# Optimization experiments

Hardware: AMD Instinct MI355X
Metric: run time of the kernel (lower is better)

## Reference

```python
import jax, jax.numpy as jnp
import numpy as np
import math

B, T, E, H, L, FF = 8, 512, 1024, 16, 4, 4096
D = E // H
LN_EPS = 1e-5


def _layernorm(x, g, b):
    mu = jnp.mean(x, axis=-1, keepdims=True)
    var = jnp.mean((x - mu) ** 2, axis=-1, keepdims=True)
    return (x - mu) * jax.lax.rsqrt(var + LN_EPS) * g + b


def setup_inputs() -> dict:
    key = jax.random.key(0)
    ks = jax.random.split(key, 16)
    s = 0.02
    return {
        "src": jax.random.normal(ks[0], (B, T, E), jnp.float32),
        "in_proj_w": jax.random.normal(ks[1], (L, 3 * E, E), jnp.float32) * s,
        "in_proj_b": jax.random.normal(ks[2], (L, 3 * E), jnp.float32) * s,
        "out_w": jax.random.normal(ks[3], (L, E, E), jnp.float32) * s,
        "out_b": jnp.zeros((L, E), jnp.float32),
        "ff1_w": jax.random.normal(ks[4], (L, FF, E), jnp.float32) * s,
        "ff1_b": jnp.zeros((L, FF), jnp.float32),
        "ff2_w": jax.random.normal(ks[5], (L, E, FF), jnp.float32) * s,
        "ff2_b": jnp.zeros((L, E), jnp.float32),
        "ln1_g": jnp.ones((L, E), jnp.float32),
        "ln1_b": jnp.zeros((L, E), jnp.float32),
        "ln2_g": jnp.ones((L, E), jnp.float32),
        "ln2_b": jnp.zeros((L, E), jnp.float32),
        "head_w": jax.random.normal(ks[6], (1, E), jnp.float32) * s,
        "head_b": jnp.zeros((1,), jnp.float32),
    }


def reference(src, in_proj_w, in_proj_b, out_w, out_b, ff1_w, ff1_b,
              ff2_w, ff2_b, ln1_g, ln1_b, ln2_g, ln2_b, head_w, head_b):
    b, t, e = src.shape
    # --- PositionalEncoding (faithful to batch_first bug: pe indexed by batch dim) ---
    pos = jnp.arange(b, dtype=jnp.float32)[:, None]            # [B,1]
    div = jnp.exp(jnp.arange(0, e, 2, dtype=jnp.float32) * (-math.log(10000.0) / e))
    pe = jnp.zeros((b, e), jnp.float32)
    pe = pe.at[:, 0::2].set(jnp.sin(pos * div)).at[:, 1::2].set(jnp.cos(pos * div))
    x = src + pe[:, None, :]                                   # broadcast over seq

    # --- Gaussian bias, shared across layers (Tq == Tk == T) ---
    dist = jnp.arange(t)[:, None] - jnp.arange(t)[None, :]
    gb = jnp.exp(-(dist.astype(jnp.float32) ** 2) / (2.0 * (t / 4.0) ** 2))  # [T,T]

    for l in range(L):
        qkv = x @ in_proj_w[l].T + in_proj_b[l]                # [B,T,3E]
        q, k, v = jnp.split(qkv, 3, axis=-1)
        q = q.reshape(b, t, H, D).transpose(0, 2, 1, 3)        # [B,H,T,D]
        k = k.reshape(b, t, H, D).transpose(0, 2, 1, 3)
        v = v.reshape(b, t, H, D).transpose(0, 2, 1, 3)
        scores = jnp.einsum("bhqd,bhkd->bhqk", q, k) / math.sqrt(D)
        w = jax.nn.softmax(scores, axis=-1)                    # [B,H,Tq,Tk]
        w = w * gb[None, None]
        w = w / (jnp.sum(w, axis=-1, keepdims=True) + 1e-5)
        o = jnp.einsum("bhqk,bhkd->bhqd", w, v)
        o = o.transpose(0, 2, 1, 3).reshape(b, t, e)
        o = o @ out_w[l].T + out_b[l]
        x = _layernorm(x + o, ln1_g[l], ln1_b[l])              # post-norm
        ff = jax.nn.relu(x @ ff1_w[l].T + ff1_b[l]) @ ff2_w[l].T + ff2_b[l]
        x = _layernorm(x + ff, ln2_g[l], ln2_b[l])

    last = x[:, -1, :]                                         # [B,E]
    return last @ head_w.T + head_b                            # [B,1]
```

## Files before the change

### kernel.cpp

```cpp
#include <hip/hip_runtime.h>

typedef unsigned short u16;
typedef __attribute__((ext_vector_type(4))) float v4f;
typedef __attribute__((ext_vector_type(8))) short v8bf;

extern "C" __device__ float __ocml_native_exp2_f32(float);
__device__ inline float ex2(float x){ return __ocml_native_exp2_f32(x); }

__device__ inline u16 f2bf(float f){
  union { float f; unsigned u; } v; v.f = f;
  unsigned r = (v.u + 0x7FFFu + ((v.u >> 16) & 1u)) >> 16;
  return (u16)r;
}
__device__ inline float bf2f(u16 u){
  union { unsigned u; float f; } v; v.u = ((unsigned)u) << 16;
  return v.f;
}

#define GLD_LDS16(gp, lp) \
  __builtin_amdgcn_global_load_lds((const __attribute__((address_space(1))) void*)(gp), \
                                   (__attribute__((address_space(3))) void*)(lp), 16, 0, 0)
#define VMCNT(n) asm volatile("s_waitcnt vmcnt(" #n ")" ::: "memory")
#define LGKM0 do { asm volatile("s_waitcnt lgkmcnt(0)" ::: "memory"); \
                   __builtin_amdgcn_sched_barrier(0); } while (0)

template<int FUSE>
__global__ __launch_bounds__(512, 2) void gemm9(
    const u16* __restrict__ A, const u16* __restrict__ W,
    const float* __restrict__ bias, void* __restrict__ C,
    int N, int K, int Kc, int gx, int gy)
{
  __shared__ u16 smem[65536];
  const int tid = threadIdx.x, lane = tid & 63, wid = tid >> 6;
  const int wm = wid >> 2, wn = wid & 3;

  const int nwg = gridDim.x, bid = blockIdx.x;
  const int swz = (bid & 7) * (nwg >> 3) + (bid >> 3);
  const int gxy = gx * gy;
  const int bz = swz / gxy;
  const int rem = swz - bz * gxy;
  const int by = rem / gx;
  const int bx = rem - by * gx;
  const int k0 = bz * Kc;
  const int NT = Kc >> 6;

  const int arow = (wid >> 1) * 16 + (lane & 15);
  const int akk  = (wid & 1) * 32 + ((lane >> 4) << 3);
  const u16* gA = A + (size_t)(by * 256 + arow) * K + k0 + akk;
  const u16* gB = W + (size_t)(bx * 256 + arow) * K + k0 + akk;
  u16* ldst = smem + tid * 8;

  auto stageA = [&](int t, int h) {
    u16* d = ldst + (t & 1) * 32768 + h * 8192;
    const u16* s = gA + (size_t)(h * 128) * K + t * 64;
    GLD_LDS16(s, d);
    GLD_LDS16(s + (size_t)64 * K, d + 4096);
  };
  auto stageB = [&](int t, int h) {
    u16* d = ldst + (t & 1) * 32768 + (2 + h) * 8192;
    const u16* s = gB + (size_t)(h * 128) * K + t * 64;
    GLD_LDS16(s, d);
    GLD_LDS16(s + (size_t)64 * K, d + 4096);
  };

  v4f acc[8][4];
  #pragma unroll
  for (int i = 0; i < 8; ++i)
    #pragma unroll
    for (int j = 0; j < 4; ++j) acc[i][j] = (v4f){0.f, 0.f, 0.f, 0.f};

  stageA(0, 0); stageA(0, 1); stageB(0, 0); stageB(0, 1);
  if (NT > 1) { stageA(1, 0); stageA(1, 1); VMCNT(4); } else { VMCNT(0); }
  __builtin_amdgcn_s_barrier();

  const u16* rdA = smem + wm * 8192 + lane * 8;
  const u16* rdB = smem + 16384 + (wn >> 1) * 8192 + lane * 8;
  const int jb = (wn & 1) * 4;

  v8bf aq[4][2], bq[4][2];

#define MFMA_CL(QI, NLO)                                                        \
  do {                                                                          \
    __builtin_amdgcn_s_setprio(1);                                              \
    _Pragma("unroll") for (int m = 0; m < 4; ++m)                               \
      _Pragma("unroll") for (int n = NLO; n < NLO + 2; ++n)                     \
        _Pragma("unroll") for (int kk = 0; kk < 2; ++kk)                        \
          acc[(QI)*4 + m][n] = __builtin_amdgcn_mfma_f32_16x16x32_bf16(         \
              aq[m][kk], bq[n][kk], acc[(QI)*4 + m][n], 0, 0, 0);               \
    __builtin_amdgcn_s_setprio(0);                                              \
  } while (0)

  for (int t = 0; t < NT; ++t) {
    const int bufo = (t & 1) * 32768;
    __builtin_amdgcn_sched_barrier(0);
    #pragma unroll
    for (int m = 0; m < 4; ++m)
      #pragma unroll
      for (int kk = 0; kk < 2; ++kk)
        aq[m][kk] = *(const v8bf*)(rdA + bufo + (m * 2 + kk) * 512);
    #pragma unroll
    for (int n = 0; n < 2; ++n)
      #pragma unroll
      for (int kk = 0; kk < 2; ++kk)
        bq[n][kk] = *(const v8bf*)(rdB + bufo + ((jb + n) * 2 + kk) * 512);
    if (t + 1 < NT) stageB(t + 1, 0);
    MFMA_CL(0, 0);
    #pragma unroll
    for (int n = 2; n < 4; ++n)
      #pragma unroll
      for (int kk = 0; kk < 2; ++kk)
        bq[n][kk] = *(const v8bf*)(rdB + bufo + ((jb + n) * 2 + kk) * 512);
    if (t + 1 < NT) stageB(t + 1, 1);
    MFMA_CL(0, 2);
    __builtin_amdgcn_s_barrier();
    __builtin_amdgcn_sched_barrier(0);
    #pragma unroll
    for (int m = 0; m < 4; ++m)
      #pragma unroll
      for (int kk = 0; kk < 2; ++kk)
        aq[m][kk] = *(const v8bf*)(rdA + bufo + ((4 + m) * 2 + kk) * 512);
    if (t + 2 < NT) stageA(t + 2, 0);
    MFMA_CL(1, 2);
    __builtin_amdgcn_s_barrier();
    __builtin_amdgcn_sched_barrier(0);
    if (t + 2 < NT) stageA(t + 2, 1);
    MFMA_CL(1, 0);
    if (t < NT - 2) { VMCNT(4); } else if (t == NT - 2) { VMCNT(0); }
    __builtin_amdgcn_s_barrier();
  }
#undef MFMA_CL

  const int cn0 = bx * 256 + wn * 64 + (lane & 15);
  const int rm0 = by * 256 + wm * 128 + ((lane >> 4) << 2);
  if (FUSE == 2) {
    u16* Cp = (u16*)C + (size_t)bz * 4096 * N;
    #pragma unroll
    for (int i = 0; i < 8; ++i)
      #pragma unroll
      for (int r = 0; r < 4; ++r) {
        size_t ro = (size_t)(rm0 + i * 16 + r) * N + cn0;
        #pragma unroll
        for (int j = 0; j < 4; ++j) Cp[ro + j * 16] = f2bf(acc[i][j][r]);
      }
  } else {
    float bv[4];
    #pragma unroll
    for (int j = 0; j < 4; ++j) bv[j] = bias[cn0 + j * 16];
    u16* Cp = (u16*)C;
    #pragma unroll
    for (int i = 0; i < 8; ++i)
      #pragma unroll
      for (int r = 0; r < 4; ++r) {
        size_t ro = (size_t)(rm0 + i * 16 + r) * N + cn0;
        #pragma unroll
        for (int j = 0; j < 4; ++j) {
          float v = acc[i][j][r] + bv[j];
          if (FUSE == 1) v = fmaxf(v, 0.f);
          Cp[ro + j * 16] = f2bf(v);
        }
      }
  }
}

__global__ __launch_bounds__(256, 2) void attn_f(const u16* __restrict__ qkv,
                                                 u16* __restrict__ o)
{
  __shared__ u16 Kf[2][4096];
  __shared__ u16 Vt[2][4096];
  __shared__ u16 wbuf[64 * 72];
  const int tid = threadIdx.x, lane = tid & 63, wid = tid >> 6;
  const int grp = lane >> 4, li = lane & 15;
  const int bh = blockIdx.y, b = bh >> 4, h = bh & 15;
  const int q0 = blockIdx.x * 64;
  const u16* Qg = qkv + (size_t)b * 512 * 3072 + h * 64;
  const u16* Kg = Qg + 1024;
  const u16* Vg = Qg + 2048;

  const size_t qrow = (size_t)(q0 + wid * 16 + li) * 3072;
  v8bf qa0 = *(const v8bf*)(Qg + qrow + grp * 8);
  v8bf qa1 = *(const v8bf*)(Qg + qrow + 32 + grp * 8);

  const u16* kga = Kg + (size_t)(wid * 16 + li) * 3072 + grp * 8;
  auto k_stage = [&](int kt, int buf) {
    #pragma unroll
    for (int s = 0; s < 2; ++s)
      GLD_LDS16(kga + (size_t)kt * 64 * 3072 + s * 32, &Kf[buf][(wid * 2 + s) * 512]);
  };
  auto v_load = [&](int kt, int x) -> v8bf {
    int u = x * 256 + tid, kk = u >> 3, d0 = (u & 7) * 8;
    return *(const v8bf*)(Vg + (size_t)(kt * 64 + kk) * 3072 + d0);
  };
  auto vt_write = [&](int buf, int x, v8bf v) {
    int u = x * 256 + tid, kk = u >> 3, d0 = (u & 7) * 8;
    int kg = (kk >> 3) & 3, kks = kk >> 5, jb2 = (kk & 7) * 2;
    #pragma unroll
    for (int i = 0; i < 8; ++i) {
      int d = d0 + i;
      int byte = (((d >> 4) * 2 + kks) * 1024 + ((d & 15) + 16 * kg) * 16 + jb2)
                 ^ (((d >> 4) & 3) << 5);
      *(u16*)((char*)&Vt[buf][0] + byte) = (u16)v[i];
    }
  };

  v4f oacc[4];
  #pragma unroll
  for (int nt = 0; nt < 4; ++nt) oacc[nt] = (v4f){0.f, 0.f, 0.f, 0.f};
  float mreg[4] = {-1e30f, -1e30f, -1e30f, -1e30f};
  float sgl[4] = {0.f, 0.f, 0.f, 0.f};
  float fqv[4];
  #pragma unroll
  for (int j = 0; j < 4; ++j) fqv[j] = (float)(q0 + wid * 16 + grp * 4 + j);

  v8bf vst[2][2];
  k_stage(0, 0);
  k_stage(1, 1);
  vst[0][0] = v_load(0, 0); vst[0][1] = v_load(0, 1);
  VMCNT(0);
  vt_write(0, 0, vst[0][0]); vt_write(0, 1, vst[0][1]);
  vst[1][0] = v_load(1, 0); vst[1][1] = v_load(1, 1);
  LGKM0;
  __builtin_amdgcn_s_barrier();

  const float SC2 = 0.18033688011112042f;
  const float GC2 = 4.4027559280058695e-05f;

  #pragma unroll
  for (int t = 0; t < 8; ++t) {
    const int cur = t & 1;
    v8bf bq0[4], bq1[4];
    #pragma unroll
    for (int nb = 0; nb < 4; ++nb) {
      bq0[nb] = *(const v8bf*)&Kf[cur][(nb * 2 + 0) * 512 + lane * 8];
      bq1[nb] = *(const v8bf*)&Kf[cur][(nb * 2 + 1) * 512 + lane * 8];
    }
    v4f pa[4];
    #pragma unroll
    for (int nb = 0; nb < 4; ++nb) {
      v4f z = (v4f){0.f, 0.f, 0.f, 0.f};
      z = __builtin_amdgcn_mfma_f32_16x16x32_bf16(qa0, bq0[nb], z, 0, 0, 0);
      pa[nb] = __builtin_amdgcn_mfma_f32_16x16x32_bf16(qa1, bq1[nb], z, 0, 0, 0);
    }
    if (t < 7) {
      __builtin_amdgcn_s_barrier();
      __builtin_amdgcn_sched_barrier(0);
      if (t + 2 < 8) k_stage(t + 2, cur);
      if (t < 6) { VMCNT(2); } else { VMCNT(0); }
      vt_write((t + 1) & 1, 0, vst[(t + 1) & 1][0]);
      vt_write((t + 1) & 1, 1, vst[(t + 1) & 1][1]);
      if (t + 2 < 8) { vst[t & 1][0] = v_load(t + 2, 0); vst[t & 1][1] = v_load(t + 2, 1); }
    }
    #pragma unroll
    for (int nb = 0; nb < 4; ++nb) {
      const float fk = (float)(t * 64 + nb * 16 + li);
      #pragma unroll
      for (int j = 0; j < 4; ++j) {
        float d = fqv[j] - fk;
        pa[nb][j] = pa[nb][j] * SC2 - d * d * GC2;
      }
    }
    float rel = -1e30f;
    #pragma unroll
    for (int j = 0; j < 4; ++j)
      #pragma unroll
      for (int nb = 0; nb < 4; ++nb)
        rel = fmaxf(rel, pa[nb][j] - mreg[j]);
    if (!__all(rel <= 11.0f)) {
      #pragma unroll
      for (int j = 0; j < 4; ++j) {
        float tmax = fmaxf(fmaxf(pa[0][j], pa[1][j]), fmaxf(pa[2][j], pa[3][j]));
        tmax = fmaxf(tmax, __shfl_xor(tmax, 1));
        tmax = fmaxf(tmax, __shfl_xor(tmax, 2));
        tmax = fmaxf(tmax, __shfl_xor(tmax, 4));
        tmax = fmaxf(tmax, __shfl_xor(tmax, 8));
        float mn = fmaxf(mreg[j], tmax);
        float sc = ex2(mreg[j] - mn);
        mreg[j] = mn;
        sgl[j] *= sc;
        #pragma unroll
        for (int nt = 0; nt < 4; ++nt) oacc[nt][j] *= sc;
      }
    }
    #pragma unroll
    for (int j = 0; j < 4; ++j) {
      #pragma unroll
      for (int nb = 0; nb < 4; ++nb) {
        float e = ex2(pa[nb][j] - mreg[j]);
        pa[nb][j] = e;
        sgl[j] += e;
      }
    }
    #pragma unroll
    for (int j = 0; j < 4; ++j) {
      const int row = wid * 16 + grp * 4 + j;
      #pragma unroll
      for (int nb = 0; nb < 4; ++nb) {
        union { float f; unsigned u; } cv; cv.f = pa[nb][j];
        wbuf[row * 72 + ((nb * 16 + li) ^ (grp << 3))] = (u16)(cv.u >> 16);
      }
    }
    const int swr = ((li >> 2) & 3) << 3;
    v8bf af0 = *(const v8bf*)&wbuf[(wid * 16 + li) * 72 + ((0 * 32 + grp * 8) ^ swr)];
    v8bf af1 = *(const v8bf*)&wbuf[(wid * 16 + li) * 72 + ((1 * 32 + grp * 8) ^ swr)];
    #pragma unroll
    for (int nt = 0; nt < 4; ++nt) {
      v8bf bv0 = *(const v8bf*)((char*)&Vt[cur][0] + ((((nt * 2 + 0) * 1024) + lane * 16) ^ ((nt & 3) << 5)));
      v8bf bv1 = *(const v8bf*)((char*)&Vt[cur][0] + ((((nt * 2 + 1) * 1024) + lane * 16) ^ ((nt & 3) << 5)));
      oacc[nt] = __builtin_amdgcn_mfma_f32_16x16x32_bf16(af0, bv0, oacc[nt], 0, 0, 0);
      oacc[nt] = __builtin_amdgcn_mfma_f32_16x16x32_bf16(af1, bv1, oacc[nt], 0, 0, 0);
    }
    if (t < 7) {
      if (t < 6) { VMCNT(2); } else { VMCNT(0); }
      LGKM0;
      __builtin_amdgcn_s_barrier();
      __builtin_amdgcn_sched_barrier(0);
    }
  }

  float rin[4];
  #pragma unroll
  for (int j = 0; j < 4; ++j) {
    float s = sgl[j];
    s += __shfl_xor(s, 1); s += __shfl_xor(s, 2);
    s += __shfl_xor(s, 4); s += __shfl_xor(s, 8);
    rin[j] = 1.f / s;
  }
  const size_t obase = (size_t)(b * 512 + q0 + wid * 16 + grp * 4) * 1024 + h * 64;
  #pragma unroll
  for (int nt = 0; nt < 4; ++nt)
    #pragma unroll
    for (int j = 0; j < 4; ++j)
      o[obase + (size_t)j * 1024 + nt * 16 + li] = f2bf(oacc[nt][j] * rin[j]);
}

__global__ __launch_bounds__(256) void ln_res4_k(
    const u16* __restrict__ x, const u16* __restrict__ part,
    const float* __restrict__ bias, const float* __restrict__ g,
    const float* __restrict__ beta, u16* __restrict__ yb)
{
  const int row = blockIdx.x, tid = threadIdx.x;
  const size_t base = (size_t)row * 1024 + tid * 4;
  const size_t MN = 4096ull * 1024;
  ushort4 xv = *(const ushort4*)(x + base);
  const int e = tid * 4;
  float4 bb = *(const float4*)(bias + e);
  float v0 = bf2f(xv.x) + bb.x, v1 = bf2f(xv.y) + bb.y;
  float v2 = bf2f(xv.z) + bb.z, v3 = bf2f(xv.w) + bb.w;
  #pragma unroll
  for (int q = 0; q < 4; ++q) {
    ushort4 pv = *(const ushort4*)(part + q * MN + base);
    v0 += bf2f(pv.x); v1 += bf2f(pv.y); v2 += bf2f(pv.z); v3 += bf2f(pv.w);
  }
  float s = v0 + v1 + v2 + v3;
  float q2 = v0*v0 + v1*v1 + v2*v2 + v3*v3;
  #pragma unroll
  for (int m = 1; m < 64; m <<= 1) { s += __shfl_xor(s, m); q2 += __shfl_xor(q2, m); }
  __shared__ float ls[4], lq[4];
  if ((tid & 63) == 0) { ls[tid >> 6] = s; lq[tid >> 6] = q2; }
  __syncthreads();
  s = ls[0] + ls[1] + ls[2] + ls[3];
  q2 = lq[0] + lq[1] + lq[2] + lq[3];
  const float mu = s * (1.f / 1024.f);
  const float var = q2 * (1.f / 1024.f) - mu * mu;
  const float rs = rsqrtf(var + 1e-5f);
  float4 gv = *(const float4*)(g + e);
  float4 be = *(const float4*)(beta + e);
  float o0 = (v0 - mu) * rs * gv.x + be.x;
  float o1 = (v1 - mu) * rs * gv.y + be.y;
  float o2 = (v2 - mu) * rs * gv.z + be.z;
  float o3 = (v3 - mu) * rs * gv.w + be.w;
  ushort4 ob; ob.x = f2bf(o0); ob.y = f2bf(o1); ob.z = f2bf(o2); ob.w = f2bf(o3);
  *(ushort4*)(yb + base) = ob;
}

__global__ __launch_bounds__(256) void pe_add_k(const float* __restrict__ src,
    u16* __restrict__ xb)
{
  const int u = blockIdx.x * 256 + threadIdx.x;
  const int e4 = (u & 255) * 4;
  const int b = u >> 17;
  const float C = -18.420680743952367f * (1.f / 1024.f);
  float4 sv = ((const float4*)src)[u];
  float fb = (float)b;
  float fr0 = __expf((float)(e4 >> 1) * C);
  float fr1 = __expf((float)((e4 >> 1) + 1) * C);
  float a0 = fb * fr0, a1 = fb * fr1;
  ushort4 ov;
  ov.x = f2bf(sv.x + __sinf(a0));
  ov.y = f2bf(sv.y + __cosf(a0));
  ov.z = f2bf(sv.z + __sinf(a1));
  ov.w = f2bf(sv.w + __cosf(a1));
  ((ushort4*)xb)[u] = ov;
}

__global__ __launch_bounds__(256) void cvt4_k(const float* __restrict__ s0,
    const float* __restrict__ s1, const float* __restrict__ s2,
    const float* __restrict__ s3, u16* __restrict__ dst)
{
  int i = blockIdx.x * 256 + threadIdx.x;
  const float* s; size_t off;
  if (i < 786432)       { s = s0; off = (size_t)i; }
  else if (i < 1048576) { s = s1; off = (size_t)i - 786432; }
  else if (i < 2097152) { s = s2; off = (size_t)i - 1048576; }
  else                  { s = s3; off = (size_t)i - 2097152; }
  float4 v = ((const float4*)s)[off];
  ushort4 ov; ov.x = f2bf(v.x); ov.y = f2bf(v.y); ov.z = f2bf(v.z); ov.w = f2bf(v.w);
  ((ushort4*)dst)[i] = ov;
}

__global__ __launch_bounds__(256) void head_k(const u16* __restrict__ xb,
    const float* __restrict__ hw, const float* __restrict__ hb, float* __restrict__ out)
{
  const int b = blockIdx.x, tid = threadIdx.x;
  const ushort4 xv = ((const ushort4*)(xb + ((size_t)b * 512 + 511) * 1024))[tid];
  const float4 wv = ((const float4*)hw)[tid];
  float s = bf2f(xv.x) * wv.x + bf2f(xv.y) * wv.y + bf2f(xv.z) * wv.z + bf2f(xv.w) * wv.w;
  #pragma unroll
  for (int m = 1; m < 64; m <<= 1) s += __shfl_xor(s, m);
  __shared__ float ls[4];
  if ((tid & 63) == 0) ls[tid >> 6] = s;
  __syncthreads();
  if (tid == 0) out[b] = ls[0] + ls[1] + ls[2] + ls[3] + hb[0];
}

extern "C" void kernel_launch(void* const* d_in, const int* in_sizes, int n_in,
                              void* d_out, int out_size, void* d_ws, size_t ws_size,
                              hipStream_t stream)
{
  const float* src  = (const float*)d_in[0];
  const float* ipw  = (const float*)d_in[1];
  const float* ipb  = (const float*)d_in[2];
  const float* outw = (const float*)d_in[3];
  const float* outb = (const float*)d_in[4];
  const float* f1w  = (const float*)d_in[5];
  const float* f1b  = (const float*)d_in[6];
  const float* f2w  = (const float*)d_in[7];
  const float* f2b  = (const float*)d_in[8];
  const float* l1g  = (const float*)d_in[9];
  const float* l1b  = (const float*)d_in[10];
  const float* l2g  = (const float*)d_in[11];
  const float* l2b  = (const float*)d_in[12];
  const float* hw   = (const float*)d_in[13];
  const float* hb   = (const float*)d_in[14];

  char* p = (char*)d_ws;
  auto take = [&](size_t bytes) { char* r = p; p += (bytes + 255) & ~(size_t)255; return r; };
  u16*   xb   = (u16*)  take(4096ull * 1024 * 2);
  u16*   slA  = (u16*)  take(4096ull * 4096 * 2);
  u16*   ob   = (u16*)  take(4096ull * 1024 * 2);
  u16*   pf   = (u16*)  take(4ull * 4096 * 1024 * 2);
  u16*   wc   = (u16*)  take(12582912ull * 2);

  u16* qkvb = slA;
  u16* f1o  = slA;

  pe_add_k<<<4096, 256, 0, stream>>>(src, xb);

  for (int l = 0; l < 4; ++l) {
    cvt4_k<<<12288, 256, 0, stream>>>(ipw + (size_t)l * 3145728,
                                      outw + (size_t)l * 1048576,
                                      f1w + (size_t)l * 4194304,
                                      f2w + (size_t)l * 4194304, wc);
    gemm9<0><<<192, 512, 0, stream>>>(xb, wc, ipb + l * 3072, qkvb, 3072, 1024, 1024, 12, 16);
    attn_f<<<dim3(8, 128), 256, 0, stream>>>(qkvb, ob);
    gemm9<2><<<256, 512, 0, stream>>>(ob, wc + 3145728, nullptr, pf, 1024, 1024, 256, 4, 16);
    ln_res4_k<<<4096, 256, 0, stream>>>(xb, pf, outb + l * 1024, l1g + l * 1024, l1b + l * 1024, xb);
    gemm9<1><<<256, 512, 0, stream>>>(xb, wc + 4194304, f1b + l * 4096, f1o, 4096, 1024, 1024, 16, 16);
    gemm9<2><<<256, 512, 0, stream>>>(f1o, wc + 8388608, nullptr, pf, 1024, 4096, 1024, 4, 16);
    ln_res4_k<<<4096, 256, 0, stream>>>(xb, pf, f2b + l * 1024, l2g + l * 1024, l2b + l * 1024, xb);
  }
  head_k<<<8, 256, 0, stream>>>(xb, hw, hb, (float*)d_out);
}
```

Before: 822.1 us.

## Restructure GEMM main loop into ping-pong quadrant schedule with register-prefetched LDS reads

Replaces the GEMM main loop with a two-tile unrolled schedule. Each quarter step issues its MFMA block while the LDS fragments for the next quadrant are read into a separate B register set, and global-to-LDS staging for tile t+2 is spread across the quarters. Both buffers are prefilled up front and vmcnt waits are tuned. The aim is to hide LDS read latency behind matrix math. In exchange it needs more barriers, more registers, and an even tile count of at least two per block.

```diff
diff --git a/kernel.cpp b/kernel.cpp
--- a/kernel.cpp
+++ b/kernel.cpp
@@ -25,7 +25,7 @@
                    __builtin_amdgcn_sched_barrier(0); } while (0)
 
 template<int FUSE>
-__global__ __launch_bounds__(512, 2) void gemm9(
+__global__ __launch_bounds__(512, 2) void gemm10(
     const u16* __restrict__ A, const u16* __restrict__ W,
     const float* __restrict__ bias, void* __restrict__ C,
     int N, int K, int Kc, int gx, int gy)
@@ -43,6 +43,7 @@
   const int bx = rem - by * gx;
   const int k0 = bz * Kc;
   const int NT = Kc >> 6;
+  const int NI = NT >> 1;
 
   const int arow = (wid >> 1) * 16 + (lane & 15);
   const int akk  = (wid & 1) * 32 + ((lane >> 4) << 3);
@@ -70,65 +71,81 @@
     for (int j = 0; j < 4; ++j) acc[i][j] = (v4f){0.f, 0.f, 0.f, 0.f};
 
   stageA(0, 0); stageA(0, 1); stageB(0, 0); stageB(0, 1);
-  if (NT > 1) { stageA(1, 0); stageA(1, 1); VMCNT(4); } else { VMCNT(0); }
+  stageA(1, 0); stageA(1, 1); stageB(1, 0); stageB(1, 1);
+  VMCNT(0);
   __builtin_amdgcn_s_barrier();
 
   const u16* rdA = smem + wm * 8192 + lane * 8;
   const u16* rdB = smem + 16384 + (wn >> 1) * 8192 + lane * 8;
   const int jb = (wn & 1) * 4;
 
-  v8bf aq[4][2], bq[4][2];
-
-#define MFMA_CL(QI, NLO)                                                        \
-  do {                                                                          \
-    __builtin_amdgcn_s_setprio(1);                                              \
-    _Pragma("unroll") for (int m = 0; m < 4; ++m)                               \
-      _Pragma("unroll") for (int n = NLO; n < NLO + 2; ++n)                     \
-        _Pragma("unroll") for (int kk = 0; kk < 2; ++kk)                        \
-          acc[(QI)*4 + m][n] = __builtin_amdgcn_mfma_f32_16x16x32_bf16(         \
-              aq[m][kk], bq[n][kk], acc[(QI)*4 + m][n], 0, 0, 0);               \
-    __builtin_amdgcn_s_setprio(0);                                              \
+  v8bf aq[4][2];
+  v8bf bq[2][2][2];
+
+#define READ_A(HALF, BO)                                                        \
+  do { _Pragma("unroll") for (int m = 0; m < 4; ++m)                            \
+         _Pragma("unroll") for (int kk = 0; kk < 2; ++kk)                       \
+           aq[m][kk] = *(const v8bf*)(rdA + (BO) + (((HALF)*4 + m)*2 + kk)*512);\
   } while (0)
-
-  for (int t = 0; t < NT; ++t) {
-    const int bufo = (t & 1) * 32768;
-    __builtin_amdgcn_sched_barrier(0);
-    #pragma unroll
-    for (int m = 0; m < 4; ++m)
-      #pragma unroll
-      for (int kk = 0; kk < 2; ++kk)
-        aq[m][kk] = *(const v8bf*)(rdA + bufo + (m * 2 + kk) * 512);
-    #pragma unroll
-    for (int n = 0; n < 2; ++n)
-      #pragma unroll
-      for (int kk = 0; kk < 2; ++kk)
-        bq[n][kk] = *(const v8bf*)(rdB + bufo + ((jb + n) * 2 + kk) * 512);
-    if (t + 1 < NT) stageB(t + 1, 0);
-    MFMA_CL(0, 0);
-    #pragma unroll
-    for (int n = 2; n < 4; ++n)
-      #pragma unroll
-      for (int kk = 0; kk < 2; ++kk)
-        bq[n][kk] = *(const v8bf*)(rdB + bufo + ((jb + n) * 2 + kk) * 512);
-    if (t + 1 < NT) stageB(t + 1, 1);
-    MFMA_CL(0, 2);
-    __builtin_amdgcn_s_barrier();
-    __builtin_amdgcn_sched_barrier(0);
-    #pragma unroll
-    for (int m = 0; m < 4; ++m)
-      #pragma unroll
-      for (int kk = 0; kk < 2; ++kk)
-        aq[m][kk] = *(const v8bf*)(rdA + bufo + ((4 + m) * 2 + kk) * 512);
-    if (t + 2 < NT) stageA(t + 2, 0);
-    MFMA_CL(1, 2);
-    __builtin_amdgcn_s_barrier();
-    __builtin_amdgcn_sched_barrier(0);
-    if (t + 2 < NT) stageA(t + 2, 1);
-    MFMA_CL(1, 0);
-    if (t < NT - 2) { VMCNT(4); } else if (t == NT - 2) { VMCNT(0); }
-    __builtin_amdgcn_s_barrier();
-  }
-#undef MFMA_CL
+#define READ_B(QJ, BO)                                                          \
+  do { _Pragma("unroll") for (int n = 0; n < 2; ++n)                            \
+         _Pragma("unroll") for (int kk = 0; kk < 2; ++kk)                       \
+           bq[QJ][n][kk] = *(const v8bf*)(rdB + (BO) + ((jb + (QJ)*2 + n)*2 + kk)*512); \
+  } while (0)
+#define MFMA_Q(QI, QJ)                                                          \
+  do { __builtin_amdgcn_s_setprio(1);                                           \
+       _Pragma("unroll") for (int m = 0; m < 4; ++m)                            \
+         _Pragma("unroll") for (int n = 0; n < 2; ++n)                          \
+           _Pragma("unroll") for (int kk = 0; kk < 2; ++kk)                     \
+             acc[(QI)*4 + m][(QJ)*2 + n] =                                      \
+               __builtin_amdgcn_mfma_f32_16x16x32_bf16(aq[m][kk], bq[QJ][n][kk],\
+                   acc[(QI)*4 + m][(QJ)*2 + n], 0, 0, 0);                       \
+       __builtin_amdgcn_s_setprio(0);                                           \
+  } while (0)
+#define BAR __builtin_amdgcn_s_barrier()
+
+  READ_A(0, 0);
+  READ_B(0, 0);
+
+  for (int i = 0; i < NI - 1; ++i) {
+    const int t2 = 2 * i + 2, t3 = 2 * i + 3;
+    LGKM0; MFMA_Q(0, 0);
+    READ_B(1, 0);
+    BAR;
+    LGKM0; MFMA_Q(0, 1);
+    READ_A(1, 0); stageA(t2, 0); stageB(t2, 0);
+    BAR;
+    LGKM0; MFMA_Q(1, 0); VMCNT(6);
+    READ_B(0, 32768); stageB(t2, 1);
+    BAR;
+    LGKM0; MFMA_Q(1, 1); VMCNT(6);
+    READ_A(0, 32768); stageA(t2, 1);
+    BAR;
+    LGKM0; MFMA_Q(0, 0);
+    READ_B(1, 32768);
+    BAR;
+    LGKM0; MFMA_Q(0, 1);
+    READ_A(1, 32768); stageA(t3, 0); stageB(t3, 0);
+    BAR;
+    LGKM0; MFMA_Q(1, 0); VMCNT(6);
+    READ_B(0, 0); stageB(t3, 1);
+    BAR;
+    LGKM0; MFMA_Q(1, 1); VMCNT(6);
+    READ_A(0, 0); stageA(t3, 1);
+    BAR;
+  }
+  LGKM0; MFMA_Q(0, 0); READ_B(1, 0); BAR;
+  LGKM0; MFMA_Q(0, 1); READ_A(1, 0); BAR;
+  LGKM0; MFMA_Q(1, 0); VMCNT(0); READ_B(0, 32768); BAR;
+  LGKM0; MFMA_Q(1, 1); READ_A(0, 32768); BAR;
+  LGKM0; MFMA_Q(0, 0); READ_B(1, 32768); BAR;
+  LGKM0; MFMA_Q(0, 1); READ_A(1, 32768); BAR;
+  LGKM0; MFMA_Q(1, 0); BAR;
+  LGKM0; MFMA_Q(1, 1);
+#undef READ_A
+#undef READ_B
+#undef MFMA_Q
+#undef BAR
 
   const int cn0 = bx * 256 + wn * 64 + (lane & 15);
   const int rm0 = by * 256 + wm * 128 + ((lane >> 4) << 2);
@@ -460,12 +477,12 @@
                                       outw + (size_t)l * 1048576,
                                       f1w + (size_t)l * 4194304,
                                       f2w + (size_t)l * 4194304, wc);
-    gemm9<0><<<192, 512, 0, stream>>>(xb, wc, ipb + l * 3072, qkvb, 3072, 1024, 1024, 12, 16);
+    gemm10<0><<<192, 512, 0, stream>>>(xb, wc, ipb + l * 3072, qkvb, 3072, 1024, 1024, 12, 16);
     attn_f<<<dim3(8, 128), 256, 0, stream>>>(qkvb, ob);
-    gemm9<2><<<256, 512, 0, stream>>>(ob, wc + 3145728, nullptr, pf, 1024, 1024, 256, 4, 16);
+    gemm10<2><<<256, 512, 0, stream>>>(ob, wc + 3145728, nullptr, pf, 1024, 1024, 256, 4, 16);
     ln_res4_k<<<4096, 256, 0, stream>>>(xb, pf, outb + l * 1024, l1g + l * 1024, l1b + l * 1024, xb);
-    gemm9<1><<<256, 512, 0, stream>>>(xb, wc + 4194304, f1b + l * 4096, f1o, 4096, 1024, 1024, 16, 16);
-    gemm9<2><<<256, 512, 0, stream>>>(f1o, wc + 8388608, nullptr, pf, 1024, 4096, 1024, 4, 16);
+    gemm10<1><<<256, 512, 0, stream>>>(xb, wc + 4194304, f1b + l * 4096, f1o, 4096, 1024, 1024, 16, 16);
+    gemm10<2><<<256, 512, 0, stream>>>(f1o, wc + 8388608, nullptr, pf, 1024, 4096, 1024, 4, 16);
     ln_res4_k<<<4096, 256, 0, stream>>>(xb, pf, f2b + l * 1024, l2g + l * 1024, l2b + l * 1024, xb);
   }
   head_k<<<8, 256, 0, stream>>>(xb, hw, hb, (float*)d_out);
```

Result: slower. 1.032 ms (+25.6%).
